# Kernel optimization log

Hardware: AMD Instinct MI355X
Metric: run time of the kernel (lower is better)

The kernel has to match this reference:

```python
import jax, jax.numpy as jnp
import numpy as np
from jax import lax

H = 20  # hidden size hardcoded in BayesianNN


def setup_inputs() -> dict:
    key = jax.random.key(0)
    ks = jax.random.split(key, 8)
    B, T, D = 256, 2048, 32
    x = jax.random.normal(ks[0], (B, T, D), dtype=jnp.float32)
    w_ih_mu = jax.random.normal(ks[1], (D, 4 * H), dtype=jnp.float32) * 0.1
    w_ih_rho = jnp.full((D, 4 * H), -3.0, dtype=jnp.float32)
    w_ih_eps = jax.random.normal(ks[2], (D, 4 * H), dtype=jnp.float32)
    w_hh_mu = jax.random.normal(ks[3], (H, 4 * H), dtype=jnp.float32) * 0.1
    w_hh_rho = jnp.full((H, 4 * H), -3.0, dtype=jnp.float32)
    w_hh_eps = jax.random.normal(ks[4], (H, 4 * H), dtype=jnp.float32)
    b_mu = jnp.zeros((4 * H,), dtype=jnp.float32)
    b_rho = jnp.full((4 * H,), -3.0, dtype=jnp.float32)
    b_eps = jax.random.normal(ks[5], (4 * H,), dtype=jnp.float32)
    w_lin = jax.random.normal(ks[6], (H, 1), dtype=jnp.float32) * 0.1
    b_lin = jnp.zeros((1,), dtype=jnp.float32)
    return {"x": x, "w_ih_mu": w_ih_mu, "w_ih_rho": w_ih_rho, "w_ih_eps": w_ih_eps,
            "w_hh_mu": w_hh_mu, "w_hh_rho": w_hh_rho, "w_hh_eps": w_hh_eps,
            "b_mu": b_mu, "b_rho": b_rho, "b_eps": b_eps,
            "w_lin": w_lin, "b_lin": b_lin}


def _sample(mu, rho, eps):
    # blitz TrainableRandomDistribution: sigma = log1p(exp(rho))
    return mu + jnp.log1p(jnp.exp(rho)) * eps


def reference(x, w_ih_mu, w_ih_rho, w_ih_eps, w_hh_mu, w_hh_rho, w_hh_eps,
              b_mu, b_rho, b_eps, w_lin, b_lin):
    w_ih = _sample(w_ih_mu, w_ih_rho, w_ih_eps)   # (D, 4H)
    w_hh = _sample(w_hh_mu, w_hh_rho, w_hh_eps)   # (H, 4H)
    bias = _sample(b_mu, b_rho, b_eps)            # (4H,)
    B = x.shape[0]
    # precompute the input-to-gate projection for all timesteps at once
    xg = jnp.einsum('btd,dg->btg', x, w_ih) + bias  # (B, T, 4H)

    def step(carry, xg_t):
        h, c = carry
        gates = xg_t + h @ w_hh                   # (B, 4H)
        i, f, g, o = jnp.split(gates, 4, axis=-1)
        i = jax.nn.sigmoid(i)
        f = jax.nn.sigmoid(f)
        g = jnp.tanh(g)
        o = jax.nn.sigmoid(o)
        c = f * c + i * g
        h = o * jnp.tanh(c)
        return (h, c), h

    h0 = jnp.zeros((B, H), dtype=x.dtype)
    c0 = jnp.zeros((B, H), dtype=x.dtype)
    (_, _), hs = lax.scan(step, (h0, c0), jnp.swapaxes(xg, 0, 1))  # hs: (T, B, H)
    h_seq = jnp.swapaxes(hs, 0, 1)                # (B, T, H)
    out = h_seq @ w_lin + b_lin                   # (B, T, 1)
    return out
```

## Files before the change

kernel.cpp:

```cpp
#include <hip/hip_runtime.h>
#include <hip/hip_bf16.h>
#include <math.h>

#define TSEQ 2048
#define DIN  32
#define HID  20
#define G4   80
#define TILE 16
#define NT   (TSEQ / TILE)
#define L2E  1.44269504088896340736f

#if __has_builtin(__builtin_amdgcn_exp2f)
#define EXP2(x) __builtin_amdgcn_exp2f(x)
#else
#define EXP2(x) __expf((x) * 0.69314718055994531f)
#endif

__device__ __forceinline__ float rl(float v, int l) {
    return __int_as_float(__builtin_amdgcn_readlane(__float_as_int(v), l));
}

__device__ __forceinline__ float sig2(float xs) {
    return __builtin_amdgcn_rcpf(1.0f + EXP2(-xs));
}

__device__ __forceinline__ float xhalf(float v) {
    float a = v, b = v;
    asm("v_permlane32_swap_b32 %0, %1" : "+v"(a), "+v"(b));
    return (a + b) - v;
}

__device__ __forceinline__ float samp(const float* mu, const float* rho,
                                      const float* eps, int i) {
    return mu[i] + log1pf(__expf(rho[i])) * eps[i];
}

__global__ __launch_bounds__(128, 1) void blstm_kernel(
    const float* __restrict__ x,
    const float* __restrict__ wih_mu, const float* __restrict__ wih_rho, const float* __restrict__ wih_eps,
    const float* __restrict__ whh_mu, const float* __restrict__ whh_rho, const float* __restrict__ whh_eps,
    const float* __restrict__ bmu,    const float* __restrict__ brho,    const float* __restrict__ beps,
    const float* __restrict__ wlin,   const float* __restrict__ blin,
    float* __restrict__ out)
{
    __shared__ __align__(16) float lds_xg[2][TILE * G4];
    __shared__ __align__(16) float lds_x[TILE * DIN];
    __shared__ __align__(16) float hist[64 * HID];

    const int tid  = threadIdx.x;
    const int lane = tid & 63;
    const int b    = blockIdx.x;
    const float* xrow = x + (size_t)b * TSEQ * DIN;
    float* outp = out + (size_t)b * TSEQ;

    if (tid < 64) {
        const int p  = lane >> 5;
        const int k  = lane & 31;
        const int ke = (k < HID) ? k : (HID - 1);
        const int g1 = p * 40 + ke;
        const int g2 = g1 + HID;
        const float aAct = p ? 2.0f : 1.0f;
        const float cAct = 1.0f - aAct;
        const float sc1 = aAct * L2E;
        const float sc2 = L2E;

        float w1[HID], w2[HID];
#pragma unroll
        for (int j = 0; j < HID; ++j) {
            w1[j] = samp(whh_mu, whh_rho, whh_eps, j * G4 + g1) * sc1;
            w2[j] = samp(whh_mu, whh_rho, whh_eps, j * G4 + g2) * sc2;
        }
        const int coff = p * 40 + ke * 2;

        float h = 0.0f, c = 0.0f;
        for (int kt = 0; kt < NT; ++kt) {
            __syncthreads();
            const float* xg = lds_xg[kt & 1];
            float2 xgr[TILE];
#pragma unroll
            for (int r = 0; r < TILE; ++r)
                xgr[r] = *(const float2*)&xg[r * G4 + coff];

#pragma unroll
            for (int ti = 0; ti < TILE; ++ti) {
                float hj[HID];
#pragma unroll
                for (int j = 0; j < HID; ++j) hj[j] = rl(h, j);

                float d1a = xgr[ti].x, d2a = xgr[ti].y;
                float d1b = 0.0f, d2b = 0.0f;
#pragma unroll
                for (int j = 0; j < HID; j += 2) {
                    d1a = fmaf(hj[j],     w1[j],     d1a);
                    d2a = fmaf(hj[j],     w2[j],     d2a);
                    d1b = fmaf(hj[j + 1], w1[j + 1], d1b);
                    d2b = fmaf(hj[j + 1], w2[j + 1], d2b);
                }
                const float d1 = d1a + d1b;
                const float d2 = d2a + d2b;

                const float s1   = sig2(d1);
                const float act1 = fmaf(s1, aAct, cAct);
                const float act2 = sig2(d2);

                const float og1 = xhalf(act1);
                const float og2 = xhalf(act2);

                c = fmaf(act2, c, act1 * og1);
                const float tc = fmaf(2.0f, sig2(c * (2.0f * L2E)), -1.0f);
                h = og2 * tc;

                const int t = kt * TILE + ti;
                if (lane < HID) hist[(t & 63) * HID + lane] = h;
            }
        }
        __syncthreads();
    } else {
        const int cA = lane;
        const int cB = 64 + (lane & 15);
        const float scA = ((cA >= 40 && cA < 60) ? 2.0f : 1.0f) * L2E;
        const float scB = L2E;

        float wA[DIN], wB[DIN];
#pragma unroll
        for (int d = 0; d < DIN; ++d) {
            wA[d] = samp(wih_mu, wih_rho, wih_eps, d * G4 + cA) * scA;
            wB[d] = samp(wih_mu, wih_rho, wih_eps, d * G4 + cB) * scB;
        }
        const float biasA = samp(bmu, brho, beps, cA) * scA;
        const float biasB = samp(bmu, brho, beps, cB) * scB;

        const int posA = ((cA >= 40) ? 40 : 0) + (cA % 20) * 2 + ((cA / 20) & 1);
        const int posB = ((cB >= 40) ? 40 : 0) + (cB % 20) * 2 + ((cB / 20) & 1);
        const int qs   = (lane >> 4) * 4;

        float wl[HID];
#pragma unroll
        for (int j = 0; j < HID; ++j) wl[j] = wlin[j];
        const float bl = blin[0];

        auto produce = [&](int kt) {
            const float* xu = xrow + kt * TILE * DIN;
            float* xgb = lds_xg[kt & 1];
            {
                const float4* src = (const float4*)xu;
                float4 v0 = src[lane * 2 + 0];
                float4 v1 = src[lane * 2 + 1];
                ((float4*)lds_x)[lane * 2 + 0] = v0;
                ((float4*)lds_x)[lane * 2 + 1] = v1;
            }
#pragma unroll
            for (int s = 0; s < TILE; ++s) {
                float a0 = 0.0f, a1 = 0.0f;
#pragma unroll
                for (int d = 0; d < 16; ++d) {
                    a0 = fmaf(xu[s * DIN + d],      wA[d],      a0);
                    a1 = fmaf(xu[s * DIN + d + 16], wA[d + 16], a1);
                }
                xgb[s * G4 + posA] = biasA + a0 + a1;
            }
#pragma unroll
            for (int jj = 0; jj < 4; ++jj) {
                const int s = qs + jj;
                const float4* xr = (const float4*)&lds_x[s * DIN];
                float a0 = 0.0f, a1 = 0.0f;
#pragma unroll
                for (int q = 0; q < 4; ++q) {
                    const float4 u0 = xr[q], u1 = xr[q + 4];
                    a0 = fmaf(u0.x, wB[q * 4 + 0],      a0);
                    a0 = fmaf(u0.y, wB[q * 4 + 1],      a0);
                    a0 = fmaf(u0.z, wB[q * 4 + 2],      a0);
                    a0 = fmaf(u0.w, wB[q * 4 + 3],      a0);
                    a1 = fmaf(u1.x, wB[16 + q * 4 + 0], a1);
                    a1 = fmaf(u1.y, wB[16 + q * 4 + 1], a1);
                    a1 = fmaf(u1.z, wB[16 + q * 4 + 2], a1);
                    a1 = fmaf(u1.w, wB[16 + q * 4 + 3], a1);
                }
                xgb[s * G4 + posB] = biasB + a0 + a1;
            }
        };

        auto flush = [&](int ft) {
            if (lane < TILE) {
                const int t = ft * TILE + lane;
                const float4* hr = (const float4*)&hist[(t & 63) * HID];
                const float4 r0 = hr[0], r1 = hr[1], r2 = hr[2], r3 = hr[3], r4 = hr[4];
                float acc = bl;
                acc = fmaf(r0.x, wl[0],  acc); acc = fmaf(r0.y, wl[1],  acc);
                acc = fmaf(r0.z, wl[2],  acc); acc = fmaf(r0.w, wl[3],  acc);
                acc = fmaf(r1.x, wl[4],  acc); acc = fmaf(r1.y, wl[5],  acc);
                acc = fmaf(r1.z, wl[6],  acc); acc = fmaf(r1.w, wl[7],  acc);
                acc = fmaf(r2.x, wl[8],  acc); acc = fmaf(r2.y, wl[9],  acc);
                acc = fmaf(r2.z, wl[10], acc); acc = fmaf(r2.w, wl[11], acc);
                acc = fmaf(r3.x, wl[12], acc); acc = fmaf(r3.y, wl[13], acc);
                acc = fmaf(r3.z, wl[14], acc); acc = fmaf(r3.w, wl[15], acc);
                acc = fmaf(r4.x, wl[16], acc); acc = fmaf(r4.y, wl[17], acc);
                acc = fmaf(r4.z, wl[18], acc); acc = fmaf(r4.w, wl[19], acc);
                outp[t] = acc;
            }
        };

        produce(0);
        for (int kt = 0; kt < NT; ++kt) {
            __syncthreads();
            if (kt + 1 < NT) produce(kt + 1);
            if (kt >= 1)     flush(kt - 1);
        }
        __syncthreads();
        flush(NT - 1);
    }
}

extern "C" void kernel_launch(void* const* d_in, const int* in_sizes, int n_in,
                              void* d_out, int out_size, void* d_ws, size_t ws_size,
                              hipStream_t stream) {
    const float* x       = (const float*)d_in[0];
    const float* wih_mu  = (const float*)d_in[1];
    const float* wih_rho = (const float*)d_in[2];
    const float* wih_eps = (const float*)d_in[3];
    const float* whh_mu  = (const float*)d_in[4];
    const float* whh_rho = (const float*)d_in[5];
    const float* whh_eps = (const float*)d_in[6];
    const float* bmu     = (const float*)d_in[7];
    const float* brho    = (const float*)d_in[8];
    const float* beps    = (const float*)d_in[9];
    const float* wlin    = (const float*)d_in[10];
    const float* blin    = (const float*)d_in[11];
    float* out = (float*)d_out;

    const int B = in_sizes[0] / (TSEQ * DIN);

    blstm_kernel<<<B, 128, 0, stream>>>(x, wih_mu, wih_rho, wih_eps,
                                        whh_mu, whh_rho, whh_eps,
                                        bmu, brho, beps, wlin, blin, out);
}
```

Measured before the change: 418.8 us.

## Split input projection into a parallel kernel and recurrence-only kernel via workspace

```diff
diff --git a/kernel.cpp b/kernel.cpp
--- a/kernel.cpp
+++ b/kernel.cpp
@@ -8,6 +8,8 @@
 #define G4   80
 #define TILE 16
 #define NT   (TSEQ / TILE)
+#define CHUNK 256
+#define NCHUNK (TSEQ / CHUNK)
 #define L2E  1.44269504088896340736f
 
 #if __has_builtin(__builtin_amdgcn_exp2f)
@@ -16,6 +18,8 @@
 #define EXP2(x) __expf((x) * 0.69314718055994531f)
 #endif
 
+typedef unsigned int uint2v __attribute__((ext_vector_type(2)));
+
 __device__ __forceinline__ float rl(float v, int l) {
     return __int_as_float(__builtin_amdgcn_readlane(__float_as_int(v), l));
 }
@@ -25,9 +29,14 @@
 }
 
 __device__ __forceinline__ float xhalf(float v) {
-    float a = v, b = v;
-    asm("v_permlane32_swap_b32 %0, %1" : "+v"(a), "+v"(b));
-    return (a + b) - v;
+#if __has_builtin(__builtin_amdgcn_permlane32_swap)
+    uint2v r = __builtin_amdgcn_permlane32_swap(__float_as_uint(v),
+                                                __float_as_uint(v),
+                                                false, false);
+    return (__uint_as_float(r.x) + __uint_as_float(r.y)) - v;
+#else
+    return __shfl_xor(v, 32);
+#endif
 }
 
 __device__ __forceinline__ float samp(const float* mu, const float* rho,
@@ -35,7 +44,160 @@
     return mu[i] + log1pf(__expf(rho[i])) * eps[i];
 }
 
-__global__ __launch_bounds__(128, 1) void blstm_kernel(
+__global__ __launch_bounds__(64, 1) void xg_kernel(
+    const float* __restrict__ x,
+    const float* __restrict__ wih_mu, const float* __restrict__ wih_rho, const float* __restrict__ wih_eps,
+    const float* __restrict__ bmu,    const float* __restrict__ brho,    const float* __restrict__ beps,
+    float* __restrict__ xg_ws)
+{
+    const int lane = threadIdx.x;
+    const int b    = blockIdx.x / NCHUNK;
+    const int ch   = blockIdx.x % NCHUNK;
+    const float* xu = x + ((size_t)b * TSEQ + (size_t)ch * CHUNK) * DIN;
+    float* xgo = xg_ws + ((size_t)b * TSEQ + (size_t)ch * CHUNK) * G4;
+
+    const int cA = lane;
+    const int cB = 64 + (lane & 15);
+    const float scA = ((cA >= 40 && cA < 60) ? 2.0f : 1.0f) * L2E;
+    const float scB = L2E;
+
+    float wA[DIN], wB[DIN];
+#pragma unroll
+    for (int d = 0; d < DIN; ++d) {
+        wA[d] = samp(wih_mu, wih_rho, wih_eps, d * G4 + cA) * scA;
+        wB[d] = samp(wih_mu, wih_rho, wih_eps, d * G4 + cB) * scB;
+    }
+    const float biasA = samp(bmu, brho, beps, cA) * scA;
+    const float biasB = samp(bmu, brho, beps, cB) * scB;
+
+    const int posA = ((cA >= 40) ? 40 : 0) + (cA % 20) * 2 + ((cA / 20) & 1);
+    const int posB = 40 + (cB % 20) * 2 + 1;
+
+#pragma unroll 4
+    for (int s = 0; s < CHUNK; ++s) {
+        const float* xs = xu + s * DIN;
+        float a0 = 0.f, a1 = 0.f, b0 = 0.f, b1 = 0.f;
+#pragma unroll
+        for (int d = 0; d < 16; ++d) {
+            const float xe = xs[d], xo = xs[d + 16];
+            a0 = fmaf(xe, wA[d],      a0);
+            a1 = fmaf(xo, wA[d + 16], a1);
+            b0 = fmaf(xe, wB[d],      b0);
+            b1 = fmaf(xo, wB[d + 16], b1);
+        }
+        xgo[s * G4 + posA] = biasA + a0 + a1;
+        if (lane < 16) xgo[s * G4 + posB] = biasB + b0 + b1;
+    }
+}
+
+__global__ __launch_bounds__(64, 1) void rec_kernel(
+    const float* __restrict__ xg_ws,
+    const float* __restrict__ whh_mu, const float* __restrict__ whh_rho, const float* __restrict__ whh_eps,
+    const float* __restrict__ wlin,   const float* __restrict__ blin,
+    float* __restrict__ out)
+{
+    __shared__ __align__(16) float hist[64 * HID];
+
+    const int lane = threadIdx.x;
+    const int b    = blockIdx.x;
+    const int p  = lane >> 5;
+    const int k  = lane & 31;
+    const int ke = (k < HID) ? k : (HID - 1);
+    const int g1 = p * 40 + ke;
+    const int g2 = g1 + HID;
+    const float aAct = p ? 2.0f : 1.0f;
+    const float cAct = 1.0f - aAct;
+    const float sc1 = aAct * L2E;
+    const float sc2 = L2E;
+
+    float w1[HID], w2[HID];
+#pragma unroll
+    for (int j = 0; j < HID; ++j) {
+        w1[j] = samp(whh_mu, whh_rho, whh_eps, j * G4 + g1) * sc1;
+        w2[j] = samp(whh_mu, whh_rho, whh_eps, j * G4 + g2) * sc2;
+    }
+    const int coff = p * 40 + ke * 2;
+
+    float wl[HID];
+#pragma unroll
+    for (int j = 0; j < HID; ++j) wl[j] = wlin[j];
+    const float bl = blin[0];
+
+    const float* xgb = xg_ws + (size_t)b * TSEQ * G4;
+    float* outp = out + (size_t)b * TSEQ;
+
+    float h = 0.0f, c = 0.0f;
+    float2 xa[TILE], xb[TILE];
+
+    auto loadt = [&](float2* dst, int kt) {
+        const float* rowp = xgb + (size_t)kt * TILE * G4 + coff;
+#pragma unroll
+        for (int s = 0; s < TILE; ++s)
+            dst[s] = *(const float2*)(rowp + s * G4);
+    };
+
+    auto steps = [&](const float2* xr, int kt) {
+#pragma unroll
+        for (int ti = 0; ti < TILE; ++ti) {
+            float hj[HID];
+#pragma unroll
+            for (int j = 0; j < HID; ++j) hj[j] = rl(h, j);
+
+            float d1a = xr[ti].x, d2a = xr[ti].y;
+            float d1b = 0.0f, d2b = 0.0f;
+#pragma unroll
+            for (int j = 0; j < HID; j += 2) {
+                d1a = fmaf(hj[j],     w1[j],     d1a);
+                d2a = fmaf(hj[j],     w2[j],     d2a);
+                d1b = fmaf(hj[j + 1], w1[j + 1], d1b);
+                d2b = fmaf(hj[j + 1], w2[j + 1], d2b);
+            }
+            const float d1 = d1a + d1b;
+            const float d2 = d2a + d2b;
+
+            const float s1   = sig2(d1);
+            const float act1 = fmaf(s1, aAct, cAct);
+            const float act2 = sig2(d2);
+
+            const float og1 = xhalf(act1);
+            const float og2 = xhalf(act2);
+
+            c = fmaf(act2, c, act1 * og1);
+            const float tc = fmaf(2.0f, sig2(c * (2.0f * L2E)), -1.0f);
+            h = og2 * tc;
+
+            const int t = kt * TILE + ti;
+            if (lane < HID) hist[(t & 63) * HID + lane] = h;
+
+            if ((t & 63) == 63) {
+                const float4* hr = (const float4*)&hist[lane * HID];
+                const float4 r0 = hr[0], r1 = hr[1], r2 = hr[2], r3 = hr[3], r4 = hr[4];
+                float acc = bl;
+                acc = fmaf(r0.x, wl[0],  acc); acc = fmaf(r0.y, wl[1],  acc);
+                acc = fmaf(r0.z, wl[2],  acc); acc = fmaf(r0.w, wl[3],  acc);
+                acc = fmaf(r1.x, wl[4],  acc); acc = fmaf(r1.y, wl[5],  acc);
+                acc = fmaf(r1.z, wl[6],  acc); acc = fmaf(r1.w, wl[7],  acc);
+                acc = fmaf(r2.x, wl[8],  acc); acc = fmaf(r2.y, wl[9],  acc);
+                acc = fmaf(r2.z, wl[10], acc); acc = fmaf(r2.w, wl[11], acc);
+                acc = fmaf(r3.x, wl[12], acc); acc = fmaf(r3.y, wl[13], acc);
+                acc = fmaf(r3.z, wl[14], acc); acc = fmaf(r3.w, wl[15], acc);
+                acc = fmaf(r4.x, wl[16], acc); acc = fmaf(r4.y, wl[17], acc);
+                acc = fmaf(r4.z, wl[18], acc); acc = fmaf(r4.w, wl[19], acc);
+                outp[(t - 63) + lane] = acc;
+            }
+        }
+    };
+
+    loadt(xa, 0);
+    for (int kt = 0; kt < NT; kt += 2) {
+        loadt(xb, kt + 1);
+        steps(xa, kt);
+        if (kt + 2 < NT) loadt(xa, kt + 2);
+        steps(xb, kt + 1);
+    }
+}
+
+__global__ __launch_bounds__(128, 1) void blstm_fused(
     const float* __restrict__ x,
     const float* __restrict__ wih_mu, const float* __restrict__ wih_rho, const float* __restrict__ wih_eps,
     const float* __restrict__ whh_mu, const float* __restrict__ whh_rho, const float* __restrict__ whh_eps,
@@ -98,18 +260,14 @@
                 }
                 const float d1 = d1a + d1b;
                 const float d2 = d2a + d2b;
-
                 const float s1   = sig2(d1);
                 const float act1 = fmaf(s1, aAct, cAct);
                 const float act2 = sig2(d2);
-
                 const float og1 = xhalf(act1);
                 const float og2 = xhalf(act2);
-
                 c = fmaf(act2, c, act1 * og1);
                 const float tc = fmaf(2.0f, sig2(c * (2.0f * L2E)), -1.0f);
                 h = og2 * tc;
-
                 const int t = kt * TILE + ti;
                 if (lane < HID) hist[(t & 63) * HID + lane] = h;
             }
@@ -129,7 +287,6 @@
         }
         const float biasA = samp(bmu, brho, beps, cA) * scA;
         const float biasB = samp(bmu, brho, beps, cB) * scB;
-
         const int posA = ((cA >= 40) ? 40 : 0) + (cA % 20) * 2 + ((cA / 20) & 1);
         const int posB = ((cB >= 40) ? 40 : 0) + (cB % 20) * 2 + ((cB / 20) & 1);
         const int qs   = (lane >> 4) * 4;
@@ -229,8 +386,17 @@
     float* out = (float*)d_out;
 
     const int B = in_sizes[0] / (TSEQ * DIN);
-
-    blstm_kernel<<<B, 128, 0, stream>>>(x, wih_mu, wih_rho, wih_eps,
-                                        whh_mu, whh_rho, whh_eps,
-                                        bmu, brho, beps, wlin, blin, out);
-}
+    const size_t need = (size_t)B * TSEQ * G4 * sizeof(float);
+
+    if (ws_size >= need) {
+        xg_kernel<<<B * NCHUNK, 64, 0, stream>>>(x, wih_mu, wih_rho, wih_eps,
+                                                 bmu, brho, beps, (float*)d_ws);
+        rec_kernel<<<B, 64, 0, stream>>>((const float*)d_ws,
+                                         whh_mu, whh_rho, whh_eps,
+                                         wlin, blin, out);
+    } else {
+        blstm_fused<<<B, 128, 0, stream>>>(x, wih_mu, wih_rho, wih_eps,
+                                           whh_mu, whh_rho, whh_eps,
+                                           bmu, brho, beps, wlin, blin, out);
+    }
+}
```

Result: slower. 565.4 us (+35.0%).
